# Optimization experiments

Hardware: AMD Instinct MI355X
Metric: run time of the kernel (lower is better)

The kernel has to match this reference:

```python
import jax, jax.numpy as jnp
import numpy as np

EPS = 1e-5


def _rmsnorm(x, eps=EPS):
    return x * jax.lax.rsqrt(jnp.mean(x * x, axis=-1, keepdims=True) + eps)


def _bitlinear(x, w):
    # fla-style BitLinear: RMSNorm (no affine) -> 8-bit activation quant (STE)
    # -> ternary weight quant (STE) -> linear. w is [out, in].
    xn = _rmsnorm(x)
    s = 127.0 / jnp.clip(jnp.max(jnp.abs(xn), axis=-1, keepdims=True), 1e-5, None)
    xq = jnp.clip(jnp.round(xn * s), -128.0, 127.0) / s
    xq = xn + jax.lax.stop_gradient(xq - xn)
    ws = 1.0 / jnp.clip(jnp.mean(jnp.abs(w)), 1e-5, None)
    wq = jnp.clip(jnp.round(w * ws), -1.0, 1.0) / ws
    wq = w + jax.lax.stop_gradient(wq - w)
    return jnp.einsum('bld,od->blo', xq, wq)


def _hgrn_scan(i, f):
    # h_t = f_t * h_{t-1} + i_t along axis=2 (seq), h_0 = 0.
    def combine(a, b):
        fa, ia = a
        fb, ib = b
        return fa * fb, ia * fb + ib
    _, h = jax.lax.associative_scan(combine, (f, i), axis=2)
    return h


def _forward(hidden_states, Wi, Wf, Wg, Wo, g_norm_weight, num_heads=1):
    b, l, d = hidden_states.shape
    i = _bitlinear(hidden_states, Wi)
    f = jax.nn.sigmoid(_bitlinear(hidden_states, Wf))
    i = jax.nn.silu(i) * (1.0 - f)  # swiglu(i, 1-f)
    # [b, l, (h d)] -> [b, h, l, d_head]
    i = i.reshape(b, l, num_heads, -1).transpose(0, 2, 1, 3)
    f = f.reshape(b, l, num_heads, -1).transpose(0, 2, 1, 3)
    h = _hgrn_scan(i, f)
    h = h.transpose(0, 2, 1, 3).reshape(b, l, d)
    # FusedRMSNormSwishGate: rmsnorm(g)*weight * h*sigmoid(h)
    g = _bitlinear(hidden_states, Wg)
    o = _rmsnorm(g) * g_norm_weight * (h * jax.nn.sigmoid(h))
    return _bitlinear(o, Wo)


def setup_inputs() -> dict:
    key = jax.random.key(0)
    ks = jax.random.split(key, 5)
    B, L, D = 4, 2048, 2048
    gain = 2 ** (-2.5) * (6.0 / (2 * D)) ** 0.5  # xavier_uniform with gain 2^-2.5
    def w(k):
        return jax.random.uniform(k, (D, D), jnp.float32, -gain, gain)
    return {
        'hidden_states': jax.random.normal(ks[0], (B, L, D), jnp.float32),
        'Wi': w(ks[1]),
        'Wf': w(ks[2]),
        'Wg': w(ks[3]),
        'Wo': w(ks[4]),
        'g_norm_weight': jnp.ones((D,), jnp.float32),
    }


def reference(hidden_states, Wi, Wf, Wg, Wo, g_norm_weight):
    return _forward(hidden_states, Wi, Wf, Wg, Wo, g_norm_weight)
```

## Files before the change

kernel.cpp:

```cpp
#include <hip/hip_runtime.h>
#include <stdint.h>

#define B_DIM 4
#define L_DIM 2048
#define D_DIM 2048
#define M_DIM 8192
#define K_DIM 2048
#define N_DIM 2048
#define WELEM (D_DIM * D_DIM)
#define CHUNK 32
#define NCH (L_DIM / CHUNK)

typedef int v4i  __attribute__((ext_vector_type(4)));
typedef int v16i __attribute__((ext_vector_type(16)));
typedef unsigned short bfraw;

#define AS1 __attribute__((address_space(1)))
#define AS3 __attribute__((address_space(3)))

__device__ __forceinline__ void gl_lds16(const void* g, void* l) {
    __builtin_amdgcn_global_load_lds((AS1 void*)g, (AS3 void*)l, 16, 0, 0);
}

__device__ __forceinline__ void wg_barrier() {
    asm volatile("" ::: "memory");
    __builtin_amdgcn_s_barrier();
    asm volatile("" ::: "memory");
}

__device__ __forceinline__ float sigmoidf_(float x) { return 1.0f / (1.0f + expf(-x)); }

__device__ __forceinline__ float bf2f(bfraw u) {
    union { unsigned int i; float f; } c; c.i = ((unsigned int)u) << 16; return c.f;
}
__device__ __forceinline__ bfraw f2bf(float f) {
    union { float f; unsigned int i; } c; c.f = f;
    unsigned int lsb = (c.i >> 16) & 1;
    c.i += 0x7fffu + lsb;
    return (bfraw)(c.i >> 16);
}

__device__ __forceinline__ void store_out(float* p, float v) { *p = v; }
__device__ __forceinline__ void store_out(bfraw* p, float v) { *p = f2bf(v); }

__device__ __forceinline__ float block_sum256(float v) {
#pragma unroll
    for (int off = 32; off > 0; off >>= 1) v += __shfl_down(v, off);
    __shared__ float sb[4];
    int lane = threadIdx.x & 63, wv = threadIdx.x >> 6;
    __syncthreads();
    if (lane == 0) sb[wv] = v;
    __syncthreads();
    return sb[0] + sb[1] + sb[2] + sb[3];
}

__device__ __forceinline__ void block_sum_max256(float& s, float& m) {
#pragma unroll
    for (int off = 32; off > 0; off >>= 1) {
        s += __shfl_down(s, off);
        m = fmaxf(m, __shfl_down(m, off));
    }
    __shared__ float sb2[8];
    int lane = threadIdx.x & 63, wv = threadIdx.x >> 6;
    __syncthreads();
    if (lane == 0) { sb2[wv] = s; sb2[4 + wv] = m; }
    __syncthreads();
    s = sb2[0] + sb2[1] + sb2[2] + sb2[3];
    m = fmaxf(fmaxf(sb2[4], sb2[5]), fmaxf(sb2[6], sb2[7]));
}

__global__ void wstats1(const float* __restrict__ w0, const float* __restrict__ w1,
                        const float* __restrict__ w2, const float* __restrict__ w3,
                        float* __restrict__ wpart) {
    int w = blockIdx.x >> 7;
    int slice = blockIdx.x & 127;
    const float* W = (w == 0) ? w0 : ((w == 1) ? w1 : ((w == 2) ? w2 : w3));
    const float4* p = (const float4*)(W + (size_t)slice * (WELEM / 128));
    float s = 0.f;
    for (int i = threadIdx.x; i < (WELEM / 128 / 4); i += 256) {
        float4 v = p[i];
        s += fabsf(v.x) + fabsf(v.y) + fabsf(v.z) + fabsf(v.w);
    }
    s = block_sum256(s);
    if (threadIdx.x == 0) wpart[blockIdx.x] = s;
}

__global__ void wstats2(const float* __restrict__ wpart, float* __restrict__ wdeq) {
    int w = threadIdx.x >> 6;
    int lane = threadIdx.x & 63;
    float s = wpart[w * 128 + lane] + wpart[w * 128 + 64 + lane];
#pragma unroll
    for (int off = 32; off > 0; off >>= 1) s += __shfl_down(s, off);
    if (lane == 0) wdeq[w] = fmaxf(s * (1.0f / (float)WELEM), 1e-5f);
}

__global__ void quant_all(const float* __restrict__ w0, const float* __restrict__ w1,
                          const float* __restrict__ w2, const float* __restrict__ w3,
                          const float* __restrict__ wdeq, int8_t* __restrict__ wq,
                          const float* __restrict__ x, int8_t* __restrict__ xq,
                          float* __restrict__ adeq) {
    if (blockIdx.x < 16384) {
        size_t idx = (size_t)blockIdx.x * 256 + threadIdx.x;
        int w = (int)(idx >> 20);
        size_t g = idx & ((1u << 20) - 1);
        const float* W = (w == 0) ? w0 : ((w == 1) ? w1 : ((w == 2) ? w2 : w3));
        float inv = 1.0f / wdeq[w];
        float4 v = ((const float4*)W)[g];
        int q0 = (int)rintf(v.x * inv); q0 = q0 < -1 ? -1 : (q0 > 1 ? 1 : q0);
        int q1 = (int)rintf(v.y * inv); q1 = q1 < -1 ? -1 : (q1 > 1 ? 1 : q1);
        int q2 = (int)rintf(v.z * inv); q2 = q2 < -1 ? -1 : (q2 > 1 ? 1 : q2);
        int q3 = (int)rintf(v.w * inv); q3 = q3 < -1 ? -1 : (q3 > 1 ? 1 : q3);
        uint32_t p = (uint32_t)(q0 & 0xff) | ((uint32_t)(q1 & 0xff) << 8) |
                     ((uint32_t)(q2 & 0xff) << 16) | ((uint32_t)(q3 & 0xff) << 24);
        ((uint32_t*)(wq + (size_t)w * WELEM))[g] = p;
        return;
    }
    int row = blockIdx.x - 16384, tid = threadIdx.x;
    const float4* xr = (const float4*)(x + (size_t)row * D_DIM);
    float4 a = xr[2 * tid], b = xr[2 * tid + 1];
    float v[8] = {a.x, a.y, a.z, a.w, b.x, b.y, b.z, b.w};
    float ss = 0.f, mx = 0.f;
#pragma unroll
    for (int j = 0; j < 8; j++) { ss += v[j] * v[j]; mx = fmaxf(mx, fabsf(v[j])); }
    block_sum_max256(ss, mx);
    float inv = rsqrtf(ss * (1.0f / (float)D_DIM) + 1e-5f);
    float anc = fmaxf(mx * inv, 1e-5f);
    float s = 127.0f / anc;
    if (tid == 0) adeq[row] = anc * (1.0f / 127.0f);
    float sc = inv * s;
    int q[8];
#pragma unroll
    for (int j = 0; j < 8; j++) {
        int t = (int)rintf(v[j] * sc);
        q[j] = t < -128 ? -128 : (t > 127 ? 127 : t);
    }
    uint32_t lo = (uint32_t)(q[0] & 0xff) | ((uint32_t)(q[1] & 0xff) << 8) |
                  ((uint32_t)(q[2] & 0xff) << 16) | ((uint32_t)(q[3] & 0xff) << 24);
    uint32_t hi = (uint32_t)(q[4] & 0xff) | ((uint32_t)(q[5] & 0xff) << 8) |
                  ((uint32_t)(q[6] & 0xff) << 16) | ((uint32_t)(q[7] & 0xff) << 24);
    ((uint2*)(xq + (size_t)row * D_DIM))[tid] = make_uint2(lo, hi);
}

#define BM 128
#define BN 256
#define BKB 64

#define MFMA32(a, b, c) __builtin_amdgcn_mfma_i32_32x32x32_i8((a), (b), (c), 0, 0, 0)

template <typename OutT>
__device__ __forceinline__ void gemm_core(
    const int8_t* __restrict__ A, const int8_t* __restrict__ Bw,
    const float* __restrict__ adeq, float wsc,
    int m0, int n0, OutT* __restrict__ Cout) {
    __shared__ __align__(16) int8_t sA[2][BM * BKB];
    __shared__ __align__(16) int8_t sB[2][BN * BKB];
    int lane = threadIdx.x & 63;
    int wv = threadIdx.x >> 6;
    int wm = (wv & 1) * 64;
    int wn = (wv >> 1) * 128;
    int r32 = lane & 31;
    int h32 = lane >> 5;

    const v16i vzero = {0, 0, 0, 0, 0, 0, 0, 0, 0, 0, 0, 0, 0, 0, 0, 0};
    v16i acc[2][4];
#pragma unroll
    for (int m = 0; m < 2; m++)
#pragma unroll
        for (int j = 0; j < 4; j++) acc[m][j] = vzero;

    const int8_t* Asrc = A + (size_t)(m0 + r32) * K_DIM + h32 * 16;
    const int8_t* Bsrc = Bw + (size_t)(n0 + r32) * K_DIM + h32 * 16;
    const int ag = (wv & 1) * 2;
    const int bg = (wv >> 1) * 4;

#define STAGE(c, kt) do {                                                                  \
    gl_lds16(Asrc + (size_t)(wv * 32) * K_DIM + (kt),            &sA[c][wv * 2048]);        \
    gl_lds16(Asrc + (size_t)(wv * 32) * K_DIM + (kt) + 32,       &sA[c][wv * 2048 + 1024]); \
    gl_lds16(Bsrc + (size_t)(wv * 32) * K_DIM + (kt),            &sB[c][wv * 2048]);        \
    gl_lds16(Bsrc + (size_t)(wv * 32) * K_DIM + (kt) + 32,       &sB[c][wv * 2048 + 1024]); \
    gl_lds16(Bsrc + (size_t)((4 + wv) * 32) * K_DIM + (kt),      &sB[c][(4 + wv) * 2048]);  \
    gl_lds16(Bsrc + (size_t)((4 + wv) * 32) * K_DIM + (kt) + 32, &sB[c][(4 + wv) * 2048 + 1024]); \
  } while (0)

    STAGE(0, 0);
    STAGE(1, BKB);
    asm volatile("s_waitcnt vmcnt(6)" ::: "memory");
    wg_barrier();

    int cur = 0;
#pragma unroll 2
    for (int kt = 0; kt < K_DIM; kt += BKB) {
        v4i af[2][2], bf[4][2];
#pragma unroll
        for (int m = 0; m < 2; m++)
#pragma unroll
            for (int k = 0; k < 2; k++)
                af[m][k] = *(const v4i*)(&sA[cur][(ag + m) * 2048 + k * 1024 + lane * 16]);
        bf[0][0] = *(const v4i*)(&sB[cur][bg * 2048 + lane * 16]);
        bf[0][1] = *(const v4i*)(&sB[cur][bg * 2048 + 1024 + lane * 16]);

#pragma unroll
        for (int j = 0; j < 3; j++) {
            bf[j + 1][0] = *(const v4i*)(&sB[cur][(bg + j + 1) * 2048 + lane * 16]);
            bf[j + 1][1] = *(const v4i*)(&sB[cur][(bg + j + 1) * 2048 + 1024 + lane * 16]);
            asm volatile("s_waitcnt lgkmcnt(2)" ::: "memory");
            __builtin_amdgcn_sched_barrier(0);
            __builtin_amdgcn_s_setprio(1);
            acc[0][j] = MFMA32(af[0][0], bf[j][0], acc[0][j]);
            acc[1][j] = MFMA32(af[1][0], bf[j][0], acc[1][j]);
            acc[0][j] = MFMA32(af[0][1], bf[j][1], acc[0][j]);
            acc[1][j] = MFMA32(af[1][1], bf[j][1], acc[1][j]);
            __builtin_amdgcn_s_setprio(0);
        }
        asm volatile("s_waitcnt lgkmcnt(0)" ::: "memory");
        __builtin_amdgcn_sched_barrier(0);
        wg_barrier();
        if (kt + 2 * BKB < K_DIM) STAGE(cur, kt + 2 * BKB);
        __builtin_amdgcn_s_setprio(1);
        acc[0][3] = MFMA32(af[0][0], bf[3][0], acc[0][3]);
        acc[1][3] = MFMA32(af[1][0], bf[3][0], acc[1][3]);
        acc[0][3] = MFMA32(af[0][1], bf[3][1], acc[0][3]);
        acc[1][3] = MFMA32(af[1][1], bf[3][1], acc[1][3]);
        __builtin_amdgcn_s_setprio(0);
        if (kt + BKB < K_DIM) {
            if (kt + 2 * BKB < K_DIM)
                asm volatile("s_waitcnt vmcnt(6)" ::: "memory");
            else
                asm volatile("s_waitcnt vmcnt(0)" ::: "memory");
            wg_barrier();
        }
        cur ^= 1;
    }
#undef STAGE

#pragma unroll
    for (int m = 0; m < 2; m++) {
#pragma unroll
        for (int r = 0; r < 16; r++) {
            int rr = (r & 3) + 8 * (r >> 2) + 4 * h32;
            int row = m0 + wm + m * 32 + rr;
            float rs = adeq[row] * wsc;
            OutT* crow = Cout + (size_t)row * N_DIM + n0 + wn + r32;
#pragma unroll
            for (int j = 0; j < 4; j++) store_out(crow + j * 32, (float)acc[m][j][r] * rs);
        }
    }
}

__global__ __launch_bounds__(256, 2) void gemm_ifg(
    const int8_t* __restrict__ xq, const int8_t* __restrict__ wq,
    const float* __restrict__ adeq, const float* __restrict__ wdeq,
    bfraw* __restrict__ bufI, bfraw* __restrict__ bufF, bfraw* __restrict__ bufG) {
    int widx = blockIdx.x >> 3;
    int n0 = (blockIdx.x & 7) * BN;
    int m0 = blockIdx.y * BM;
    bfraw* outp = (widx == 0) ? bufI : ((widx == 1) ? bufF : bufG);
    gemm_core<bfraw>(xq, wq + (size_t)widx * WELEM, adeq, wdeq[widx], m0, n0, outp);
}

__global__ __launch_bounds__(256, 2) void gemm_o(
    const int8_t* __restrict__ oq, const int8_t* __restrict__ wq,
    const float* __restrict__ odeq, const float* __restrict__ wdeq,
    float* __restrict__ out) {
    gemm_core<float>(oq, wq + 3 * (size_t)WELEM, odeq, wdeq[3], blockIdx.y * BM,
                     blockIdx.x * BN, out);
}

__global__ void scan1(const bfraw* __restrict__ iL, const bfraw* __restrict__ fL,
                      float* __restrict__ Fc, float* __restrict__ Ic) {
    int idx = blockIdx.x * 256 + threadIdx.x;
    int d = idx & (D_DIM - 1);
    int c = (idx >> 11) & (NCH - 1);
    int b = idx >> 17;
    size_t base = ((size_t)(b * L_DIM + c * CHUNK)) * D_DIM + d;
    float F = 1.f, h = 0.f;
#pragma unroll 4
    for (int t = 0; t < CHUNK; t++) {
        float fr = bf2f(fL[base + (size_t)t * D_DIM]);
        float ir = bf2f(iL[base + (size_t)t * D_DIM]);
        float fv = sigmoidf_(fr);
        float iv = ir * sigmoidf_(ir) * (1.0f - fv);
        h = fv * h + iv;
        F *= fv;
    }
    size_t ci = ((size_t)b * NCH + c) * D_DIM + d;
    Fc[ci] = F;
    Ic[ci] = h;
}

__global__ void scan2(const float* __restrict__ Fc, const float* __restrict__ Ic,
                      float* __restrict__ Hc) {
    int idx = blockIdx.x * 256 + threadIdx.x;
    int d = idx & (D_DIM - 1);
    int b = idx >> 11;
    float h = 0.f;
    for (int c0 = 0; c0 < NCH; c0 += 8) {
        float F[8], I[8];
#pragma unroll
        for (int j = 0; j < 8; j++) {
            size_t ci = ((size_t)b * NCH + c0 + j) * D_DIM + d;
            F[j] = Fc[ci];
            I[j] = Ic[ci];
        }
#pragma unroll
        for (int j = 0; j < 8; j++) {
            size_t ci = ((size_t)b * NCH + c0 + j) * D_DIM + d;
            Hc[ci] = h;
            h = F[j] * h + I[j];
        }
    }
}

__global__ void scan3(const bfraw* __restrict__ iL, const bfraw* __restrict__ fL,
                      const float* __restrict__ Hc, bfraw* __restrict__ hout) {
    int idx = blockIdx.x * 256 + threadIdx.x;
    int d = idx & (D_DIM - 1);
    int c = (idx >> 11) & (NCH - 1);
    int b = idx >> 17;
    size_t base = ((size_t)(b * L_DIM + c * CHUNK)) * D_DIM + d;
    float h = Hc[((size_t)b * NCH + c) * D_DIM + d];
#pragma unroll 4
    for (int t = 0; t < CHUNK; t++) {
        size_t a = base + (size_t)t * D_DIM;
        float fr = bf2f(fL[a]);
        float ir = bf2f(iL[a]);
        float fv = sigmoidf_(fr);
        float iv = ir * sigmoidf_(ir) * (1.0f - fv);
        h = fv * h + iv;
        hout[a] = f2bf(h);
    }
}

union BF8 { uint4 u; bfraw s[8]; };

__global__ void gout_quant(const bfraw* __restrict__ gL, const bfraw* __restrict__ h,
                           const float* __restrict__ gw, int8_t* __restrict__ oq,
                           float* __restrict__ odeq) {
    int row = blockIdx.x, tid = threadIdx.x;
    BF8 g8, h8;
    g8.u = ((const uint4*)(gL + (size_t)row * D_DIM))[tid];
    float gv[8];
    float ss = 0.f;
#pragma unroll
    for (int j = 0; j < 8; j++) { gv[j] = bf2f(g8.s[j]); ss += gv[j] * gv[j]; }
    float ssg = block_sum256(ss);
    float invg = rsqrtf(ssg * (1.0f / (float)D_DIM) + 1e-5f);

    h8.u = ((const uint4*)(h + (size_t)row * D_DIM))[tid];
    const float4* wr = (const float4*)gw;
    float4 w0 = wr[2 * tid], w1 = wr[2 * tid + 1];
    float wv[8] = {w0.x, w0.y, w0.z, w0.w, w1.x, w1.y, w1.z, w1.w};
    float o[8];
    float sso = 0.f, amax = 0.f;
#pragma unroll
    for (int j = 0; j < 8; j++) {
        float hv = bf2f(h8.s[j]);
        o[j] = gv[j] * invg * wv[j] * hv * sigmoidf_(hv);
        sso += o[j] * o[j];
        amax = fmaxf(amax, fabsf(o[j]));
    }
    block_sum_max256(sso, amax);
    float invo = rsqrtf(sso * (1.0f / (float)D_DIM) + 1e-5f);
    float anc = fmaxf(amax * invo, 1e-5f);
    float s = 127.0f / anc;
    if (tid == 0) odeq[row] = anc * (1.0f / 127.0f);
    float sc = invo * s;
    int q[8];
#pragma unroll
    for (int j = 0; j < 8; j++) {
        int t = (int)rintf(o[j] * sc);
        q[j] = t < -128 ? -128 : (t > 127 ? 127 : t);
    }
    uint32_t lo = (uint32_t)(q[0] & 0xff) | ((uint32_t)(q[1] & 0xff) << 8) |
                  ((uint32_t)(q[2] & 0xff) << 16) | ((uint32_t)(q[3] & 0xff) << 24);
    uint32_t hi = (uint32_t)(q[4] & 0xff) | ((uint32_t)(q[5] & 0xff) << 8) |
                  ((uint32_t)(q[6] & 0xff) << 16) | ((uint32_t)(q[7] & 0xff) << 24);
    ((uint2*)(oq + (size_t)row * D_DIM))[tid] = make_uint2(lo, hi);
}

extern "C" void kernel_launch(void* const* d_in, const int* in_sizes, int n_in,
                              void* d_out, int out_size, void* d_ws, size_t ws_size,
                              hipStream_t stream) {
    const float* x  = (const float*)d_in[0];
    const float* Wi = (const float*)d_in[1];
    const float* Wf = (const float*)d_in[2];
    const float* Wg = (const float*)d_in[3];
    const float* Wo = (const float*)d_in[4];
    const float* gw = (const float*)d_in[5];
    float* out = (float*)d_out;

    char* ws = (char*)d_ws;
    float*  wdeq  = (float*)(ws + 0);
    float*  wpart = (float*)(ws + 256);
    float*  adeq  = (float*)(ws + 0x10000);
    float*  odeq  = (float*)(ws + 0x20000);
    int8_t* xq    = (int8_t*)(ws + 0x100000);
    int8_t* wq    = (int8_t*)(ws + 0x1100000);
    float*  Fc    = (float*)(ws + 0x2100000);
    float*  Ic    = (float*)(ws + 0x2300000);
    float*  Hc    = (float*)(ws + 0x2500000);
    bfraw*  bufI  = (bfraw*)(ws + 0x4000000);
    bfraw*  bufF  = (bfraw*)(ws + 0x6000000);
    bfraw*  bufG  = (bfraw*)(ws + 0x8000000);
    bfraw*  hbuf  = (bfraw*)(ws + 0xA000000);

    wstats1<<<512, 256, 0, stream>>>(Wi, Wf, Wg, Wo, wpart);
    wstats2<<<1, 256, 0, stream>>>(wpart, wdeq);
    quant_all<<<16384 + 8192, 256, 0, stream>>>(Wi, Wf, Wg, Wo, wdeq, wq, x, xq, adeq);

    gemm_ifg<<<dim3(24, M_DIM / BM), 256, 0, stream>>>(xq, wq, adeq, wdeq, bufI, bufF, bufG);

    scan1<<<2048, 256, 0, stream>>>(bufI, bufF, Fc, Ic);
    scan2<<<32, 256, 0, stream>>>(Fc, Ic, Hc);
    scan3<<<2048, 256, 0, stream>>>(bufI, bufF, Hc, hbuf);

    gout_quant<<<M_DIM, 256, 0, stream>>>(bufG, hbuf, gw, xq , odeq);
    gemm_o<<<dim3(N_DIM / BN, M_DIM / BM), 256, 0, stream>>>(xq , wq, odeq, wdeq, out);

    (void)in_sizes; (void)n_in; (void)out_size; (void)ws_size;
}
```

Baseline: 482.4 us.

## Restructure int8 GEMM to 256x256 tiles, 8 waves, triple-buffered LDS ping-pong

Reworks the shared int8 MFMA GEMM core to use 256x256 block tiles with 512 threads (8 waves in a 2x4 grid, each computing 128x64). LDS staging moves from double to triple buffering, and each k-step is split into two barrier-separated halves that interleave fragment loads, global-to-LDS prefetch and MFMA bursts. The aim is more reuse per loaded byte and better overlap of memory traffic with compute. In exchange it uses 96KB of LDS per block, which probably limits occupancy to one block per CU despite the launch bounds, and it adds more workgroup barriers per iteration.

```diff
diff --git a/kernel.cpp b/kernel.cpp
--- a/kernel.cpp
+++ b/kernel.cpp
@@ -141,9 +141,10 @@
     ((uint2*)(xq + (size_t)row * D_DIM))[tid] = make_uint2(lo, hi);
 }
 
-#define BM 128
-#define BN 256
+#define BM2 256
+#define BN2 256
 #define BKB 64
+#define NT (K_DIM / BKB)
 
 #define MFMA32(a, b, c) __builtin_amdgcn_mfma_i32_32x32x32_i8((a), (b), (c), 0, 0, 0)
 
@@ -152,118 +153,125 @@
     const int8_t* __restrict__ A, const int8_t* __restrict__ Bw,
     const float* __restrict__ adeq, float wsc,
     int m0, int n0, OutT* __restrict__ Cout) {
-    __shared__ __align__(16) int8_t sA[2][BM * BKB];
-    __shared__ __align__(16) int8_t sB[2][BN * BKB];
+    __shared__ __align__(16) int8_t sA[3][BM2 * BKB];
+    __shared__ __align__(16) int8_t sB[3][BN2 * BKB];
     int lane = threadIdx.x & 63;
     int wv = threadIdx.x >> 6;
-    int wm = (wv & 1) * 64;
-    int wn = (wv >> 1) * 128;
+    int wr = wv >> 2, wc = wv & 3;
     int r32 = lane & 31;
     int h32 = lane >> 5;
+    const int ag = wr * 4;
+    const int bg = wc * 2;
+    const int lb = lane * 16;
 
     const v16i vzero = {0, 0, 0, 0, 0, 0, 0, 0, 0, 0, 0, 0, 0, 0, 0, 0};
-    v16i acc[2][4];
-#pragma unroll
-    for (int m = 0; m < 2; m++)
-#pragma unroll
-        for (int j = 0; j < 4; j++) acc[m][j] = vzero;
+    v16i acc[4][2];
+#pragma unroll
+    for (int m = 0; m < 4; m++)
+#pragma unroll
+        for (int n = 0; n < 2; n++) acc[m][n] = vzero;
 
     const int8_t* Asrc = A + (size_t)(m0 + r32) * K_DIM + h32 * 16;
     const int8_t* Bsrc = Bw + (size_t)(n0 + r32) * K_DIM + h32 * 16;
-    const int ag = (wv & 1) * 2;
-    const int bg = (wv >> 1) * 4;
-
-#define STAGE(c, kt) do {                                                                  \
-    gl_lds16(Asrc + (size_t)(wv * 32) * K_DIM + (kt),            &sA[c][wv * 2048]);        \
-    gl_lds16(Asrc + (size_t)(wv * 32) * K_DIM + (kt) + 32,       &sA[c][wv * 2048 + 1024]); \
-    gl_lds16(Bsrc + (size_t)(wv * 32) * K_DIM + (kt),            &sB[c][wv * 2048]);        \
-    gl_lds16(Bsrc + (size_t)(wv * 32) * K_DIM + (kt) + 32,       &sB[c][wv * 2048 + 1024]); \
-    gl_lds16(Bsrc + (size_t)((4 + wv) * 32) * K_DIM + (kt),      &sB[c][(4 + wv) * 2048]);  \
-    gl_lds16(Bsrc + (size_t)((4 + wv) * 32) * K_DIM + (kt) + 32, &sB[c][(4 + wv) * 2048 + 1024]); \
+
+#define STG(c, kt, s) do {                                                                  \
+    gl_lds16(Asrc + (size_t)(wv * 32) * K_DIM + (kt) + (s) * 32, &sA[c][wv * 2048 + (s) * 1024]); \
+    gl_lds16(Bsrc + (size_t)(wv * 32) * K_DIM + (kt) + (s) * 32, &sB[c][wv * 2048 + (s) * 1024]); \
   } while (0)
 
-    STAGE(0, 0);
-    STAGE(1, BKB);
-    asm volatile("s_waitcnt vmcnt(6)" ::: "memory");
+#define LDF(buf, grp, s) (*(const v4i*)(&(buf)[(grp) * 2048 + (s) * 1024 + lb]))
+
+    STG(0, 0, 0);   STG(0, 0, 1);
+    STG(1, BKB, 0); STG(1, BKB, 1);
+    asm volatile("s_waitcnt vmcnt(4)" ::: "memory");
     wg_barrier();
 
     int cur = 0;
-#pragma unroll 2
-    for (int kt = 0; kt < K_DIM; kt += BKB) {
-        v4i af[2][2], bf[4][2];
-#pragma unroll
-        for (int m = 0; m < 2; m++)
-#pragma unroll
-            for (int k = 0; k < 2; k++)
-                af[m][k] = *(const v4i*)(&sA[cur][(ag + m) * 2048 + k * 1024 + lane * 16]);
-        bf[0][0] = *(const v4i*)(&sB[cur][bg * 2048 + lane * 16]);
-        bf[0][1] = *(const v4i*)(&sB[cur][bg * 2048 + 1024 + lane * 16]);
-
-#pragma unroll
-        for (int j = 0; j < 3; j++) {
-            bf[j + 1][0] = *(const v4i*)(&sB[cur][(bg + j + 1) * 2048 + lane * 16]);
-            bf[j + 1][1] = *(const v4i*)(&sB[cur][(bg + j + 1) * 2048 + 1024 + lane * 16]);
-            asm volatile("s_waitcnt lgkmcnt(2)" ::: "memory");
-            __builtin_amdgcn_sched_barrier(0);
-            __builtin_amdgcn_s_setprio(1);
-            acc[0][j] = MFMA32(af[0][0], bf[j][0], acc[0][j]);
-            acc[1][j] = MFMA32(af[1][0], bf[j][0], acc[1][j]);
-            acc[0][j] = MFMA32(af[0][1], bf[j][1], acc[0][j]);
-            acc[1][j] = MFMA32(af[1][1], bf[j][1], acc[1][j]);
-            __builtin_amdgcn_s_setprio(0);
-        }
+    for (int t = 0; t < NT; ++t) {
+        const int8_t* bA = &sA[cur][0];
+        const int8_t* bB = &sB[cur][0];
+        int c2 = cur + 2; if (c2 >= 3) c2 -= 3;
+        int kt2 = (t + 2) * BKB;
+
+        v4i a0s0 = LDF(bA, ag + 0, 0), a0s1 = LDF(bA, ag + 0, 1);
+        v4i a1s0 = LDF(bA, ag + 1, 0), a1s1 = LDF(bA, ag + 1, 1);
+        v4i b0s0 = LDF(bB, bg + 0, 0), b0s1 = LDF(bB, bg + 0, 1);
+        v4i b1s0 = LDF(bB, bg + 1, 0), b1s1 = LDF(bB, bg + 1, 1);
+        if (t + 2 < NT) STG(c2, kt2, 0);
+        wg_barrier();
         asm volatile("s_waitcnt lgkmcnt(0)" ::: "memory");
         __builtin_amdgcn_sched_barrier(0);
+        __builtin_amdgcn_s_setprio(1);
+        acc[0][0] = MFMA32(a0s0, b0s0, acc[0][0]);
+        acc[1][0] = MFMA32(a1s0, b0s0, acc[1][0]);
+        acc[0][1] = MFMA32(a0s0, b1s0, acc[0][1]);
+        acc[1][1] = MFMA32(a1s0, b1s0, acc[1][1]);
+        acc[0][0] = MFMA32(a0s1, b0s1, acc[0][0]);
+        acc[1][0] = MFMA32(a1s1, b0s1, acc[1][0]);
+        acc[0][1] = MFMA32(a0s1, b1s1, acc[0][1]);
+        acc[1][1] = MFMA32(a1s1, b1s1, acc[1][1]);
+        __builtin_amdgcn_s_setprio(0);
         wg_barrier();
-        if (kt + 2 * BKB < K_DIM) STAGE(cur, kt + 2 * BKB);
+
+        v4i a2s0 = LDF(bA, ag + 2, 0), a2s1 = LDF(bA, ag + 2, 1);
+        v4i a3s0 = LDF(bA, ag + 3, 0), a3s1 = LDF(bA, ag + 3, 1);
+        if (t + 2 < NT) {
+            STG(c2, kt2, 1);
+            asm volatile("s_waitcnt vmcnt(4)" ::: "memory");
+        } else if (t + 1 < NT) {
+            asm volatile("s_waitcnt vmcnt(0)" ::: "memory");
+        }
+        wg_barrier();
+        asm volatile("s_waitcnt lgkmcnt(0)" ::: "memory");
+        __builtin_amdgcn_sched_barrier(0);
         __builtin_amdgcn_s_setprio(1);
-        acc[0][3] = MFMA32(af[0][0], bf[3][0], acc[0][3]);
-        acc[1][3] = MFMA32(af[1][0], bf[3][0], acc[1][3]);
-        acc[0][3] = MFMA32(af[0][1], bf[3][1], acc[0][3]);
-        acc[1][3] = MFMA32(af[1][1], bf[3][1], acc[1][3]);
+        acc[2][0] = MFMA32(a2s0, b0s0, acc[2][0]);
+        acc[3][0] = MFMA32(a3s0, b0s0, acc[3][0]);
+        acc[2][1] = MFMA32(a2s0, b1s0, acc[2][1]);
+        acc[3][1] = MFMA32(a3s0, b1s0, acc[3][1]);
+        acc[2][0] = MFMA32(a2s1, b0s1, acc[2][0]);
+        acc[3][0] = MFMA32(a3s1, b0s1, acc[3][0]);
+        acc[2][1] = MFMA32(a2s1, b1s1, acc[2][1]);
+        acc[3][1] = MFMA32(a3s1, b1s1, acc[3][1]);
         __builtin_amdgcn_s_setprio(0);
-        if (kt + BKB < K_DIM) {
-            if (kt + 2 * BKB < K_DIM)
-                asm volatile("s_waitcnt vmcnt(6)" ::: "memory");
-            else
-                asm volatile("s_waitcnt vmcnt(0)" ::: "memory");
-            wg_barrier();
-        }
-        cur ^= 1;
-    }
-#undef STAGE
-
-#pragma unroll
-    for (int m = 0; m < 2; m++) {
+        wg_barrier();
+
+        cur = cur + 1; if (cur >= 3) cur = 0;
+    }
+#undef LDF
+#undef STG
+
+#pragma unroll
+    for (int m = 0; m < 4; m++) {
 #pragma unroll
         for (int r = 0; r < 16; r++) {
             int rr = (r & 3) + 8 * (r >> 2) + 4 * h32;
-            int row = m0 + wm + m * 32 + rr;
+            int row = m0 + (ag + m) * 32 + rr;
             float rs = adeq[row] * wsc;
-            OutT* crow = Cout + (size_t)row * N_DIM + n0 + wn + r32;
-#pragma unroll
-            for (int j = 0; j < 4; j++) store_out(crow + j * 32, (float)acc[m][j][r] * rs);
+            OutT* crow = Cout + (size_t)row * N_DIM + n0 + bg * 32 + r32;
+            store_out(crow,      (float)acc[m][0][r] * rs);
+            store_out(crow + 32, (float)acc[m][1][r] * rs);
         }
     }
 }
 
-__global__ __launch_bounds__(256, 2) void gemm_ifg(
+__global__ __launch_bounds__(512, 2) void gemm_ifg(
     const int8_t* __restrict__ xq, const int8_t* __restrict__ wq,
     const float* __restrict__ adeq, const float* __restrict__ wdeq,
     bfraw* __restrict__ bufI, bfraw* __restrict__ bufF, bfraw* __restrict__ bufG) {
     int widx = blockIdx.x >> 3;
-    int n0 = (blockIdx.x & 7) * BN;
-    int m0 = blockIdx.y * BM;
+    int n0 = (blockIdx.x & 7) * BN2;
+    int m0 = blockIdx.y * BM2;
     bfraw* outp = (widx == 0) ? bufI : ((widx == 1) ? bufF : bufG);
     gemm_core<bfraw>(xq, wq + (size_t)widx * WELEM, adeq, wdeq[widx], m0, n0, outp);
 }
 
-__global__ __launch_bounds__(256, 2) void gemm_o(
+__global__ __launch_bounds__(512, 2) void gemm_o(
     const int8_t* __restrict__ oq, const int8_t* __restrict__ wq,
     const float* __restrict__ odeq, const float* __restrict__ wdeq,
     float* __restrict__ out) {
-    gemm_core<float>(oq, wq + 3 * (size_t)WELEM, odeq, wdeq[3], blockIdx.y * BM,
-                     blockIdx.x * BN, out);
+    gemm_core<float>(oq, wq + 3 * (size_t)WELEM, odeq, wdeq[3], blockIdx.y * BM2,
+                     blockIdx.x * BN2, out);
 }
 
 __global__ void scan1(const bfraw* __restrict__ iL, const bfraw* __restrict__ fL,
@@ -408,14 +416,14 @@
     wstats2<<<1, 256, 0, stream>>>(wpart, wdeq);
     quant_all<<<16384 + 8192, 256, 0, stream>>>(Wi, Wf, Wg, Wo, wdeq, wq, x, xq, adeq);
 
-    gemm_ifg<<<dim3(24, M_DIM / BM), 256, 0, stream>>>(xq, wq, adeq, wdeq, bufI, bufF, bufG);
+    gemm_ifg<<<dim3(24, M_DIM / BM2), 512, 0, stream>>>(xq, wq, adeq, wdeq, bufI, bufF, bufG);
 
     scan1<<<2048, 256, 0, stream>>>(bufI, bufF, Fc, Ic);
     scan2<<<32, 256, 0, stream>>>(Fc, Ic, Hc);
     scan3<<<2048, 256, 0, stream>>>(bufI, bufF, Hc, hbuf);
 
     gout_quant<<<M_DIM, 256, 0, stream>>>(bufG, hbuf, gw, xq , odeq);
-    gemm_o<<<dim3(N_DIM / BN, M_DIM / BM), 256, 0, stream>>>(xq , wq, odeq, wdeq, out);
+    gemm_o<<<dim3(N_DIM / BN2, M_DIM / BM2), 512, 0, stream>>>(xq , wq, odeq, wdeq, out);
 
     (void)in_sizes; (void)n_in; (void)out_size; (void)ws_size;
 }
```

New measurement: 454.7 us. 5.7% less time.
